# Kernel optimization log

Hardware: AMD Instinct MI355X
Metric: run time of the kernel (lower is better)

Reference implementation:

```python
import jax, jax.numpy as jnp
import numpy as np

LATENT = 512
CIN = 512
COUT = 512
K = 3
B, H, W = 16, 64, 64

# equalized-lr multipliers (use_wscale=True, lrmul=1, gain=1)
W_MUL_CONV = (CIN * K * K) ** (-0.5)
W_MUL_DENSE = LATENT ** (-0.5)


def setup_inputs() -> dict:
    key = jax.random.key(0)
    k1, k2, k3, k4 = jax.random.split(key, 4)
    x = jax.random.normal(k1, (B, CIN, H, W), dtype=jnp.float32)
    y = jax.random.normal(k2, (B, LATENT), dtype=jnp.float32)
    dense_w = jax.random.normal(k3, (CIN, LATENT), dtype=jnp.float32)
    dense_b = jnp.ones((CIN,), dtype=jnp.float32)  # style bias, init 1 (StyleGAN2)
    weight = jax.random.normal(k4, (COUT, CIN, K, K), dtype=jnp.float32)
    return {"x": x, "y": y, "dense_w": dense_w, "dense_b": dense_b, "weight": weight}


def reference(x, y, dense_w, dense_b, weight):
    # style: s[b, cin] = (y @ dense_w.T) * w_mul + bias (linear bias_act)
    s = jnp.einsum('bl,cl->bc', y, dense_w) * W_MUL_DENSE + dense_b  # [B, Cin]

    # modulate: per-sample weights ww[b,o,i,kh,kw]
    w = weight * W_MUL_CONV
    ww = w[None] * s[:, None, :, None, None]  # [B, Cout, Cin, K, K]

    # demodulate
    d = jax.lax.rsqrt(jnp.sum(ww * ww, axis=(2, 3, 4)) + 1e-8)  # [B, Cout]
    ww = ww * d[:, :, None, None, None]

    # fused grouped conv: groups = B, VALID padding (F.conv2d default)
    b = x.shape[0]
    x_g = x.reshape(1, b * CIN, H, W)
    w_g = ww.reshape(b * COUT, CIN, K, K)
    out = jax.lax.conv_general_dilated(
        x_g, w_g,
        window_strides=(1, 1), padding='VALID',
        dimension_numbers=('NCHW', 'OIHW', 'NCHW'),
        feature_group_count=b)
    return out.reshape(b, COUT, H - K + 1, W - K + 1)
```

## Files before the change

### kernel.cpp

```cpp
#include <hip/hip_runtime.h>
#include <hip/hip_bf16.h>

#define CIN 512
#define COUT 512
#define BATCH 16
#define NP 3844
#define OW 62

#define W_MUL_DENSE 0.044194173824159216f
#define W_MUL_CONV  0.014731391274719736f

using short8  = __attribute__((ext_vector_type(8))) short;
using floatx4 = __attribute__((ext_vector_type(4))) float;
using uintx4  = __attribute__((ext_vector_type(4))) unsigned int;

__device__ __forceinline__ unsigned short f2bfu(float f) {
    unsigned u = __builtin_bit_cast(unsigned, f);
    u += 0x7FFFu + ((u >> 16) & 1u);
    return (unsigned short)(u >> 16);
}

__device__ __forceinline__ void gload_lds16(const void* g, void* l) {
    __builtin_amdgcn_global_load_lds(
        (const __attribute__((address_space(1))) void*)g,
        (__attribute__((address_space(3))) void*)l, 16, 0, 0);
}


__global__ void emc_style_kernel(const float* __restrict__ y, const float* __restrict__ dw,
                                 const float* __restrict__ db, float* __restrict__ s) {
    int idx = blockIdx.x * 256 + threadIdx.x;
    int b = idx >> 9, c = idx & 511;
    const float4* yb = (const float4*)(y + b * 512);
    const float4* wc = (const float4*)(dw + c * 512);
    float acc = 0.f;
#pragma unroll 4
    for (int l = 0; l < 128; ++l) {
        float4 a = yb[l], w4 = wc[l];
        acc += a.x * w4.x + a.y * w4.y + a.z * w4.z + a.w * w4.w;
    }
    s[idx] = acc * W_MUL_DENSE + db[c];
}

__global__ void emc_wsq_kernel(const float* __restrict__ w, float* __restrict__ wsq) {
    int idx = blockIdx.x * 256 + threadIdx.x;
    const float* p = w + (size_t)idx * 9;
    float a = 0.f;
#pragma unroll
    for (int j = 0; j < 9; ++j) a += p[j] * p[j];
    wsq[idx] = a;
}

__global__ void emc_demod_kernel(const float* __restrict__ s, const float* __restrict__ wsq,
                                 float* __restrict__ d) {
    int idx = blockIdx.x * 256 + threadIdx.x;
    int b = idx >> 9, o = idx & 511;
    const float4* sb = (const float4*)(s + b * 512);
    const float4* wo = (const float4*)(wsq + o * 512);
    float acc = 0.f;
#pragma unroll 4
    for (int l = 0; l < 128; ++l) {
        float4 a = sb[l], c = wo[l];
        acc += a.x * a.x * c.x + a.y * a.y * c.y + a.z * a.z * c.z + a.w * a.w * c.w;
    }
    d[idx] = rsqrtf(W_MUL_CONV * W_MUL_CONV * acc + 1e-8f);
}

__global__ void emc_wrepack_kernel(const float* __restrict__ w, unsigned short* __restrict__ wb) {
    int idx = blockIdx.x * 256 + threadIdx.x;
    int i = idx & 511;
    int r = idx >> 9;
    int kpos = r % 9;
    int o = r / 9;
    wb[idx] = f2bfu(w[(size_t)(o * 512 + i) * 9 + kpos]);
}


__global__ __launch_bounds__(256, 2) void emc_conv_kernel(
    const float* __restrict__ x, const unsigned short* __restrict__ wb,
    const float* __restrict__ sv, const float* __restrict__ dv,
    float* __restrict__ out) {

    __shared__ __align__(16) unsigned short smA[2][256 * 32];
    __shared__ __align__(16) unsigned short smB[260 * 40];
    __shared__ float s_s[512];
    __shared__ float s_d[256];

    int orig = blockIdx.x;
    int cpx = gridDim.x >> 3;
    int bid = (orig & 7) * cpx + (orig >> 3);

    int b = bid / 62;
    int t = bid - b * 62;
    int ot = t & 1;
    int strip = t >> 1;
    int oB = ot * 256;
    int r0 = strip * 2;

    int tid = threadIdx.x;
    int lane = tid & 63;
    int wid = tid >> 6;

    s_s[tid]       = sv[b * 512 + tid];
    s_s[tid + 256] = sv[b * 512 + 256 + tid];
    s_d[tid]       = dv[b * 512 + oB + tid];

    int sc = tid & 63;
    int sr = tid >> 6;
    const float* xrow = x + (size_t)b * (512 * 4096) + (r0 + sr) * 64 + sc;
    unsigned short* bg = smB + (sr * 64 + sc) * 40;

    const unsigned short* asrc[4];
    int adst[4];
#pragma unroll
    for (int j = 0; j < 4; ++j) {
        int row = wid * 64 + j * 16 + (lane >> 2);
        asrc[j] = wb + (size_t)(oB + row) * 4608 + (((lane & 3) ^ ((row >> 1) & 3)) << 3);
        adst[j] = (wid * 64 + j * 16) * 32;
    }

    int frc = lane & 15, q = lane >> 4;
    int wr = wid >> 1, wc = wid & 1;
    int aidx[8], bidx[4];
#pragma unroll
    for (int m = 0; m < 8; ++m) {
        int row = wr * 128 + m * 16 + frc;
        aidx[m] = row * 32 + ((q ^ ((row >> 1) & 3)) << 3);
    }
#pragma unroll
    for (int n = 0; n < 4; ++n) bidx[n] = (wc * 64 + n * 16 + frc) * 40 + q * 8;

    floatx4 acc[8][4];
#pragma unroll
    for (int m = 0; m < 8; ++m)
#pragma unroll
        for (int n = 0; n < 4; ++n) acc[m][n] = floatx4{0.f, 0.f, 0.f, 0.f};

    unsigned held[16];

    __syncthreads();

#pragma unroll
    for (int j = 0; j < 4; ++j)
        gload_lds16(asrc[j], &smA[0][adst[j]]);

#pragma unroll
    for (int sl = 0; sl < 8; ++sl) {
        const float* xp = xrow + (size_t)(sl * 4) * 4096;
        int i0 = sl * 4;
        float v0 = xp[0]         * s_s[i0];
        float v1 = xp[4096]      * s_s[i0 + 1];
        float v2 = xp[2 * 4096]  * s_s[i0 + 2];
        float v3 = xp[3 * 4096]  * s_s[i0 + 3];
        held[2 * sl]     = (unsigned)f2bfu(v0) | ((unsigned)f2bfu(v1) << 16);
        held[2 * sl + 1] = (unsigned)f2bfu(v2) | ((unsigned)f2bfu(v3) << 16);
    }
    *(uintx4*)(bg)      = uintx4{held[0],  held[1],  held[2],  held[3]};
    *(uintx4*)(bg + 8)  = uintx4{held[4],  held[5],  held[6],  held[7]};
    *(uintx4*)(bg + 16) = uintx4{held[8],  held[9],  held[10], held[11]};
    *(uintx4*)(bg + 24) = uintx4{held[12], held[13], held[14], held[15]};

    __syncthreads();

    for (int itile = 0; itile < 16; ++itile) {
        const float* xit = xrow + (size_t)(itile + 1) * 32 * 4096;
        int sbase = (itile + 1) * 32;
        int cur = itile & 1;
#pragma unroll
        for (int kpos = 0; kpos < 9; ++kpos) {
            int abuf = (cur + kpos) & 1;
            if (!(itile == 15 && kpos == 8)) {
                int kN = (kpos == 8) ? 0 : kpos + 1;
                int iN = (kpos == 8) ? itile + 1 : itile;
                int off = kN * 512 + iN * 32;
#pragma unroll
                for (int j = 0; j < 4; ++j)
                    gload_lds16(asrc[j] + off, &smA[abuf ^ 1][adst[j]]);
            }
            if (kpos < 8 && itile < 15) {
                const float* xp = xit + (size_t)(kpos * 4) * 4096;
                int i0 = sbase + kpos * 4;
                float v0 = xp[0]        * s_s[i0];
                float v1 = xp[4096]     * s_s[i0 + 1];
                float v2 = xp[2 * 4096] * s_s[i0 + 2];
                float v3 = xp[3 * 4096] * s_s[i0 + 3];
                held[2 * kpos]     = (unsigned)f2bfu(v0) | ((unsigned)f2bfu(v1) << 16);
                held[2 * kpos + 1] = (unsigned)f2bfu(v2) | ((unsigned)f2bfu(v3) << 16);
            }
            {
                int kh = kpos / 3, kw = kpos - kh * 3;
                int bo = (kh * 64 + kw) * 40;
                const unsigned short* A = smA[abuf];
                short8 bfr[4];
#pragma unroll
                for (int n = 0; n < 4; ++n) bfr[n] = *(const short8*)(smB + bidx[n] + bo);
#pragma unroll
                for (int mh = 0; mh < 2; ++mh) {
                    short8 af[4];
#pragma unroll
                    for (int mm = 0; mm < 4; ++mm) af[mm] = *(const short8*)(A + aidx[mh * 4 + mm]);
#pragma unroll
                    for (int mm = 0; mm < 4; ++mm)
#pragma unroll
                        for (int n = 0; n < 4; ++n)
                            acc[mh * 4 + mm][n] = __builtin_amdgcn_mfma_f32_16x16x32_bf16(
                                af[mm], bfr[n], acc[mh * 4 + mm][n], 0, 0, 0);
                }
            }
            if (kpos == 8) {
                __syncthreads();
                if (itile < 15) {
                    *(uintx4*)(bg)      = uintx4{held[0],  held[1],  held[2],  held[3]};
                    *(uintx4*)(bg + 8)  = uintx4{held[4],  held[5],  held[6],  held[7]};
                    *(uintx4*)(bg + 16) = uintx4{held[8],  held[9],  held[10], held[11]};
                    *(uintx4*)(bg + 24) = uintx4{held[12], held[13], held[14], held[15]};
                }
                __syncthreads();
            } else {
                __syncthreads();
            }
        }
    }

    size_t outb = (size_t)b * 512 * NP;
#pragma unroll
    for (int m = 0; m < 8; ++m) {
#pragma unroll
        for (int r = 0; r < 4; ++r) {
            int o_l = wr * 128 + m * 16 + q * 4 + r;
            float scale = W_MUL_CONV * s_d[o_l];
            size_t rb = outb + (size_t)(oB + o_l) * NP + strip * 124 + wc * OW;
#pragma unroll
            for (int n = 0; n < 4; ++n) {
                int col = n * 16 + frc;
                if (col < OW) out[rb + col] = acc[m][n][r] * scale;
            }
        }
    }
}

extern "C" void kernel_launch(void* const* d_in, const int* in_sizes, int n_in,
                              void* d_out, int out_size, void* d_ws, size_t ws_size,
                              hipStream_t stream) {
    const float* x  = (const float*)d_in[0];
    const float* y  = (const float*)d_in[1];
    const float* dw = (const float*)d_in[2];
    const float* db = (const float*)d_in[3];
    const float* w  = (const float*)d_in[4];
    float* out = (float*)d_out;

    char* ws = (char*)d_ws;
    float* s_  = (float*)ws;
    float* d_  = (float*)(ws + 32768);
    float* wsq = (float*)(ws + 65536);
    unsigned short* wb = (unsigned short*)(ws + 65536 + 1048576);

    emc_style_kernel<<<32, 256, 0, stream>>>(y, dw, db, s_);
    emc_wsq_kernel<<<1024, 256, 0, stream>>>(w, wsq);
    emc_demod_kernel<<<32, 256, 0, stream>>>(s_, wsq, d_);
    emc_wrepack_kernel<<<9216, 256, 0, stream>>>(w, wb);
    emc_conv_kernel<<<16 * 62, 256, 0, stream>>>(x, wb, s_, d_, out);
}
```

Measured before the change: 349.1 us.

## Triple-buffer weight tiles with prefetch distance two and explicit waitcnt barriers

After: 349.3 us. Within noise of the previous version (+0.1%).

```diff
diff --git a/kernel.cpp b/kernel.cpp
--- a/kernel.cpp
+++ b/kernel.cpp
@@ -81,7 +81,7 @@
     const float* __restrict__ sv, const float* __restrict__ dv,
     float* __restrict__ out) {
 
-    __shared__ __align__(16) unsigned short smA[2][256 * 32];
+    __shared__ __align__(16) unsigned short smA[3][256 * 32];
     __shared__ __align__(16) unsigned short smB[260 * 40];
     __shared__ float s_s[512];
     __shared__ float s_d[256];
@@ -138,87 +138,100 @@
 
     unsigned held[16];
 
-    __syncthreads();
-
-#pragma unroll
-    for (int j = 0; j < 4; ++j)
-        gload_lds16(asrc[j], &smA[0][adst[j]]);
-
-#pragma unroll
-    for (int sl = 0; sl < 8; ++sl) {
-        const float* xp = xrow + (size_t)(sl * 4) * 4096;
-        int i0 = sl * 4;
-        float v0 = xp[0]         * s_s[i0];
-        float v1 = xp[4096]      * s_s[i0 + 1];
-        float v2 = xp[2 * 4096]  * s_s[i0 + 2];
-        float v3 = xp[3 * 4096]  * s_s[i0 + 3];
+    auto ISSUE_A = [&](int kN, int iN, int bufsel) {
+        int off = kN * 512 + iN * 32;
+#pragma unroll
+        for (int j = 0; j < 4; ++j)
+            gload_lds16(asrc[j] + off, &smA[bufsel][adst[j]]);
+    };
+
+    auto STAGE_SLICE = [&](int itgt, int sl) {
+        const float* xp = xrow + ((size_t)itgt * 32 + sl * 4) * 4096;
+        int i0 = itgt * 32 + sl * 4;
+        float v0 = xp[0]        * s_s[i0];
+        float v1 = xp[4096]     * s_s[i0 + 1];
+        float v2 = xp[2 * 4096] * s_s[i0 + 2];
+        float v3 = xp[3 * 4096] * s_s[i0 + 3];
         held[2 * sl]     = (unsigned)f2bfu(v0) | ((unsigned)f2bfu(v1) << 16);
         held[2 * sl + 1] = (unsigned)f2bfu(v2) | ((unsigned)f2bfu(v3) << 16);
-    }
-    *(uintx4*)(bg)      = uintx4{held[0],  held[1],  held[2],  held[3]};
-    *(uintx4*)(bg + 8)  = uintx4{held[4],  held[5],  held[6],  held[7]};
-    *(uintx4*)(bg + 16) = uintx4{held[8],  held[9],  held[10], held[11]};
-    *(uintx4*)(bg + 24) = uintx4{held[12], held[13], held[14], held[15]};
+    };
+
+    auto WRITE_B = [&]() {
+        *(uintx4*)(bg)      = uintx4{held[0],  held[1],  held[2],  held[3]};
+        *(uintx4*)(bg + 8)  = uintx4{held[4],  held[5],  held[6],  held[7]};
+        *(uintx4*)(bg + 16) = uintx4{held[8],  held[9],  held[10], held[11]};
+        *(uintx4*)(bg + 24) = uintx4{held[12], held[13], held[14], held[15]};
+    };
+
+    auto COMPUTE = [&](int kpos, int bufsel) {
+        int kh = kpos / 3, kw = kpos - kh * 3;
+        int bo = (kh * 64 + kw) * 40;
+        const unsigned short* A = smA[bufsel];
+        short8 bfr[4];
+#pragma unroll
+        for (int n = 0; n < 4; ++n) bfr[n] = *(const short8*)(smB + bidx[n] + bo);
+        __builtin_amdgcn_s_setprio(1);
+#pragma unroll
+        for (int mh = 0; mh < 2; ++mh) {
+            short8 af[4];
+#pragma unroll
+            for (int mm = 0; mm < 4; ++mm) af[mm] = *(const short8*)(A + aidx[mh * 4 + mm]);
+#pragma unroll
+            for (int mm = 0; mm < 4; ++mm)
+#pragma unroll
+                for (int n = 0; n < 4; ++n)
+                    acc[mh * 4 + mm][n] = __builtin_amdgcn_mfma_f32_16x16x32_bf16(
+                        af[mm], bfr[n], acc[mh * 4 + mm][n], 0, 0, 0);
+        }
+        __builtin_amdgcn_s_setprio(0);
+    };
 
     __syncthreads();
 
-    for (int itile = 0; itile < 16; ++itile) {
-        const float* xit = xrow + (size_t)(itile + 1) * 32 * 4096;
-        int sbase = (itile + 1) * 32;
-        int cur = itile & 1;
+    ISSUE_A(0, 0, 0);
+    ISSUE_A(1, 0, 1);
+#pragma unroll
+    for (int sl = 0; sl < 8; ++sl) STAGE_SLICE(0, sl);
+    WRITE_B();
+    asm volatile("s_waitcnt vmcnt(4) lgkmcnt(0)" ::: "memory");
+    __builtin_amdgcn_s_barrier();
+
+    for (int itile = 0; itile < 15; ++itile) {
 #pragma unroll
         for (int kpos = 0; kpos < 9; ++kpos) {
-            int abuf = (cur + kpos) & 1;
-            if (!(itile == 15 && kpos == 8)) {
-                int kN = (kpos == 8) ? 0 : kpos + 1;
-                int iN = (kpos == 8) ? itile + 1 : itile;
-                int off = kN * 512 + iN * 32;
-#pragma unroll
-                for (int j = 0; j < 4; ++j)
-                    gload_lds16(asrc[j] + off, &smA[abuf ^ 1][adst[j]]);
+            if (kpos < 8) STAGE_SLICE(itile + 1, kpos);
+            {
+                int kN = (kpos + 2) % 9;
+                int iN = itile + (kpos + 2) / 9;
+                ISSUE_A(kN, iN, (kpos + 2) % 3);
             }
-            if (kpos < 8 && itile < 15) {
-                const float* xp = xit + (size_t)(kpos * 4) * 4096;
-                int i0 = sbase + kpos * 4;
-                float v0 = xp[0]        * s_s[i0];
-                float v1 = xp[4096]     * s_s[i0 + 1];
-                float v2 = xp[2 * 4096] * s_s[i0 + 2];
-                float v3 = xp[3 * 4096] * s_s[i0 + 3];
-                held[2 * kpos]     = (unsigned)f2bfu(v0) | ((unsigned)f2bfu(v1) << 16);
-                held[2 * kpos + 1] = (unsigned)f2bfu(v2) | ((unsigned)f2bfu(v3) << 16);
+            COMPUTE(kpos, kpos % 3);
+            if (kpos == 8) {
+                asm volatile("s_waitcnt vmcnt(4)" ::: "memory");
+                __builtin_amdgcn_s_barrier();
+                WRITE_B();
+                asm volatile("s_waitcnt lgkmcnt(0)" ::: "memory");
+                __builtin_amdgcn_s_barrier();
+            } else {
+                asm volatile("s_waitcnt vmcnt(4)" ::: "memory");
+                __builtin_amdgcn_s_barrier();
             }
-            {
-                int kh = kpos / 3, kw = kpos - kh * 3;
-                int bo = (kh * 64 + kw) * 40;
-                const unsigned short* A = smA[abuf];
-                short8 bfr[4];
-#pragma unroll
-                for (int n = 0; n < 4; ++n) bfr[n] = *(const short8*)(smB + bidx[n] + bo);
-#pragma unroll
-                for (int mh = 0; mh < 2; ++mh) {
-                    short8 af[4];
-#pragma unroll
-                    for (int mm = 0; mm < 4; ++mm) af[mm] = *(const short8*)(A + aidx[mh * 4 + mm]);
-#pragma unroll
-                    for (int mm = 0; mm < 4; ++mm)
-#pragma unroll
-                        for (int n = 0; n < 4; ++n)
-                            acc[mh * 4 + mm][n] = __builtin_amdgcn_mfma_f32_16x16x32_bf16(
-                                af[mm], bfr[n], acc[mh * 4 + mm][n], 0, 0, 0);
-                }
-            }
-            if (kpos == 8) {
-                __syncthreads();
-                if (itile < 15) {
-                    *(uintx4*)(bg)      = uintx4{held[0],  held[1],  held[2],  held[3]};
-                    *(uintx4*)(bg + 8)  = uintx4{held[4],  held[5],  held[6],  held[7]};
-                    *(uintx4*)(bg + 16) = uintx4{held[8],  held[9],  held[10], held[11]};
-                    *(uintx4*)(bg + 24) = uintx4{held[12], held[13], held[14], held[15]};
-                }
-                __syncthreads();
-            } else {
-                __syncthreads();
-            }
+        }
+    }
+
+#pragma unroll
+    for (int kpos = 0; kpos < 9; ++kpos) {
+        if (kpos <= 6) {
+            int kN = (kpos + 2) % 9;
+            ISSUE_A(kN, 15, (kpos + 2) % 3);
+        }
+        COMPUTE(kpos, kpos % 3);
+        if (kpos < 7) {
+            asm volatile("s_waitcnt vmcnt(4)" ::: "memory");
+            __builtin_amdgcn_s_barrier();
+        } else if (kpos == 7) {
+            asm volatile("s_waitcnt vmcnt(0)" ::: "memory");
+            __builtin_amdgcn_s_barrier();
         }
     }
 
```
